# Performance work log

Measured on AMD Instinct MI355X. Metric: run time of the kernel, lower is better.

Reference implementation:

```python
import jax, jax.numpy as jnp
import numpy as np

# Hyperparameters matching init_kwargs
DIM = 1024
HEADS = 16
MEM_HIDDEN = 512
FF_DIM = 4096
CHUNK = 128
NPERSIST = 16
ALPHA = 0.02
THETA = 0.1
ETA = 0.9
B, T = 2, 1024


def _mem_read(x, p):
    """DeepMemory forward: 2-layer MLP dim->hidden->dim with SiLU between."""
    W1, b1, W2, b2 = p
    h = jax.nn.silu(x @ W1.T + b1)
    return h @ W2.T + b2


def setup_inputs() -> dict:
    key = jax.random.key(0)
    ks = jax.random.split(key, 16)
    s = 0.02  # weight init scale
    return {
        "x": jax.random.normal(ks[0], (B, T, DIM), jnp.float32),
        "Wqkv": jax.random.normal(ks[1], (3 * DIM, DIM), jnp.float32) * s,
        "mW1": jax.random.normal(ks[2], (MEM_HIDDEN, DIM), jnp.float32) * s,
        "mb1": jnp.zeros((MEM_HIDDEN,), jnp.float32),
        "mW2": jax.random.normal(ks[3], (DIM, MEM_HIDDEN), jnp.float32) * s,
        "mb2": jnp.zeros((DIM,), jnp.float32),
        "P": jax.random.normal(ks[4], (1, NPERSIST, DIM), jnp.float32),
        "Wqkv_attn": jax.random.normal(ks[5], (3 * DIM, DIM), jnp.float32) * s,
        "Wo": jax.random.normal(ks[6], (DIM, DIM), jnp.float32) * s,
        "ffW1": jax.random.normal(ks[7], (FF_DIM, DIM), jnp.float32) * s,
        "ffb1": jnp.zeros((FF_DIM,), jnp.float32),
        "ffW2": jax.random.normal(ks[8], (DIM, FF_DIM), jnp.float32) * s,
        "ffb2": jnp.zeros((DIM,), jnp.float32),
    }


def reference(x, Wqkv, mW1, mb1, mW2, mb2, P, Wqkv_attn, Wo, ffW1, ffb1, ffW2, ffb2):
    Bb, Tt, D = x.shape
    nC = Tt // CHUNK

    # shared qkv projection (bias-free Linear)
    qkv = x @ Wqkv.T                       # [B,T,3D]
    K = qkv[..., D:2 * D]
    V = qkv[..., 2 * D:]

    # chunked test-time memory writes: k,v are detached in the torch code
    Kc = jax.lax.stop_gradient(K).reshape(Bb, nC, CHUNK, D).transpose(1, 0, 2, 3)  # [nC,B,C,D]
    Vc = jax.lax.stop_gradient(V).reshape(Bb, nC, CHUNK, D).transpose(1, 0, 2, 3)

    params0 = tuple(jax.lax.stop_gradient(p) for p in (mW1, mb1, mW2, mb2))
    mom0 = tuple(jnp.zeros_like(p) for p in params0)

    def loss_fn(p, k, v):
        return jnp.mean((_mem_read(k, p) - v) ** 2)

    def step(carry, kv):
        p, m = carry
        k, v = kv
        g = jax.grad(loss_fn)(p, k, v)
        # momentum: s = eta*s - theta*g ; weight: w = (1-alpha)*w + s
        m = tuple(ETA * mi - THETA * gi for mi, gi in zip(m, g))
        p = tuple((1.0 - ALPHA) * pi + mi for pi, mi in zip(p, m))
        return (p, m), None

    (pf, _), _ = jax.lax.scan(step, (params0, mom0), (Kc, Vc))
    pf = jax.lax.stop_gradient(pf)  # fast weights are buffers (non-differentiable)

    # memory readout tokens for the whole segment
    Q = qkv[..., :D]
    mem_tok = _mem_read(Q, pf)             # [B,T,D]

    # concatenate persistent + memory + input tokens
    tokens = jnp.concatenate([jnp.broadcast_to(P, (Bb, NPERSIST, D)), mem_tok, x], axis=1)
    N = tokens.shape[1]                    # NPERSIST + 2T
    dh = D // HEADS

    # causal multi-head attention over the concatenated sequence
    aqkv = tokens @ Wqkv_attn.T            # [B,N,3D]
    q, k, v = jnp.split(aqkv, 3, axis=-1)
    to_heads = lambda t: t.reshape(Bb, N, HEADS, dh).transpose(0, 2, 1, 3)
    q, k, v = to_heads(q), to_heads(k), to_heads(v)
    scores = jnp.einsum('bhnd,bhmd->bhnm', q, k) / jnp.sqrt(jnp.float32(dh))
    causal = jnp.tril(jnp.ones((N, N), bool))
    scores = jnp.where(causal, scores, jnp.float32(-1e9))
    attn = jax.nn.softmax(scores, axis=-1)
    o = jnp.einsum('bhnm,bhmd->bhnd', attn, v).transpose(0, 2, 1, 3).reshape(Bb, N, D)
    y = o @ Wo.T

    # feed-forward (no residual in source)
    y = jax.nn.gelu(y @ ffW1.T + ffb1) @ ffW2.T + ffb2

    # drop persistent + memory tokens, gate by a fresh memory read
    out = y[:, NPERSIST + Tt:, :]          # [B,T,D]
    newQ = (out @ Wqkv.T)[..., :D]
    return out * _mem_read(newQ, pf)
```

## Files before the change

### kernel.cpp

```cpp
#include <hip/hip_runtime.h>
#include <math.h>

#define BATCH 2
#define TSEQ 1024
#define DIMD 1024
#define NPERS 16
#define NCH 8
#define NTOK 2064
#define ETA_C 0.9f
#define THETA_C 0.1f
#define ALPHA_C 0.02f

typedef __attribute__((ext_vector_type(4))) float f32x4;
typedef __attribute__((ext_vector_type(8))) short s16x8;
typedef unsigned short u16;

__device__ __forceinline__ u16 f2bf(float f) {
    unsigned int u = __float_as_uint(f);
    return (u16)((u + 0x7fffu + ((u >> 16) & 1u)) >> 16);
}
__device__ __forceinline__ float bf2f(u16 h) { return __uint_as_float(((unsigned)h) << 16); }
__device__ __forceinline__ void split2(float v, u16& h, u16& l) {
    h = f2bf(v); l = f2bf(v - bf2f(h));
}

static const size_t oRA = 0;
static const size_t oRB = 50724864;
static const size_t oRC = 67633152;
static const size_t oRD = 80216064;
static const size_t oRE = 96993280;
static const size_t oRF = 109576192;
static const size_t oRG = 113770496;
static const size_t oRH = 117970944;

static const size_t PW1 = 0, PB1 = 524288, PW2 = 524800, PB2 = 1049088, PSZ = 1050112;

__device__ __forceinline__ void gload_lds16(const u16* g, u16* l) {
    __builtin_amdgcn_global_load_lds(
        (const __attribute__((address_space(1))) unsigned int*)g,
        (__attribute__((address_space(3))) unsigned int*)l, 16, 0, 0);
}

__device__ __forceinline__ void xcd_swizzle(int& bx, int& by) {
    int gx = gridDim.x, nwg = gx * gridDim.y;
    int lid = blockIdx.y * gx + blockIdx.x;
    int t = lid;
    if ((nwg & 7) == 0) {
        int q = nwg >> 3;
        t = (lid & 7) * q + (lid >> 3);
    }
    bx = t % gx; by = t / gx;
}

__device__ __forceinline__ void stage_tile(const u16* sp, u16* buf, int rbase,
                                           int M, int clampM, int K, int k0,
                                           int wid, int lane) {
    const int lr = lane >> 2, lc = lane & 3;
    #pragma unroll
    for (int i = 0; i < 8; ++i) {
        int r = i * 16 + lr;
        int gr = rbase + r;
        if (clampM && gr >= M) gr = M - 1;
        int g = lc ^ ((r >> 1) & 3);
        gload_lds16(sp + (size_t)gr * K + k0 + g * 8, buf + wid * 4096 + i * 512);
    }
}

__device__ __forceinline__ void stage_tile64(const u16* sp, u16* buf, int rbase,
                                             int K, int k0, int wid, int lane) {
    const int lr = lane >> 3, lc = lane & 7;
    #pragma unroll
    for (int i = 0; i < 16; ++i) {
        int r = i * 8 + lr;
        int gr = rbase + r;
        int g = lc ^ (r & 7);
        gload_lds16(sp + (size_t)gr * K + k0 + g * 8, buf + wid * 8192 + i * 512);
    }
}

template<int ACTF, int WF32, int WSPLIT, int PARTIAL>
__global__ __launch_bounds__(256)
void gemm_mfma_k(const u16* __restrict__ Ah, const u16* __restrict__ Al,
                 const u16* __restrict__ Wh, const u16* __restrict__ Wl,
                 float* __restrict__ C, u16* __restrict__ Chi, u16* __restrict__ Clo,
                 int M, int N, int K, const float* __restrict__ bias)
{
    __shared__ u16 lds[2][16384];
    const int tid = threadIdx.x;
    const int lane = tid & 63, wid = tid >> 6;
    const int wm = wid >> 1, wn = wid & 1;
    int bx, by; xcd_swizzle(bx, by);
    const int row0 = by * 128, col0 = bx * 128;

    const u16* sp = (wid == 0) ? Ah : (wid == 1) ? Al : (wid == 2) ? Wh : Wl;
    const int rbase = (wid < 2) ? row0 : col0;
    const int clampM = (wid < 2) ? 1 : 0;

    f32x4 acc[4][4] = {};
    const int frow = lane & 15, kblk = lane >> 4;

    int kbeg = 0, kend = K;
    if (PARTIAL) {
        int Kseg = K / gridDim.z;
        kbeg = blockIdx.z * Kseg;
        kend = kbeg + Kseg;
    }
    const int nt = (kend - kbeg) >> 5;

    stage_tile(sp, lds[0], rbase, M, clampM, K, kbeg, wid, lane);

    for (int t = 0; t < nt; ++t) {
        __syncthreads();
        if (t + 1 < nt)
            stage_tile(sp, lds[(t + 1) & 1], rbase, M, clampM, K, kbeg + ((t + 1) << 5), wid, lane);
        const u16* cb = lds[t & 1];

        s16x8 bh[4], bl[4];
        #pragma unroll
        for (int ni = 0; ni < 4; ++ni) {
            int br = wn * 64 + ni * 16 + frow;
            int pc = kblk ^ ((br >> 1) & 3);
            bh[ni] = *(const s16x8*)&cb[2 * 4096 + br * 32 + pc * 8];
            bl[ni] = *(const s16x8*)&cb[3 * 4096 + br * 32 + pc * 8];
        }
        #pragma unroll
        for (int mi = 0; mi < 4; ++mi) {
            int ar = wm * 64 + mi * 16 + frow;
            int pc = kblk ^ ((ar >> 1) & 3);
            s16x8 ah = *(const s16x8*)&cb[0 * 4096 + ar * 32 + pc * 8];
            s16x8 al = *(const s16x8*)&cb[1 * 4096 + ar * 32 + pc * 8];
            #pragma unroll
            for (int ni = 0; ni < 4; ++ni) {
                acc[mi][ni] = __builtin_amdgcn_mfma_f32_16x16x32_bf16(ah, bh[ni], acc[mi][ni], 0, 0, 0);
                acc[mi][ni] = __builtin_amdgcn_mfma_f32_16x16x32_bf16(ah, bl[ni], acc[mi][ni], 0, 0, 0);
                acc[mi][ni] = __builtin_amdgcn_mfma_f32_16x16x32_bf16(al, bh[ni], acc[mi][ni], 0, 0, 0);
            }
        }
    }

    const int erow = (lane >> 4) * 4, ecol = lane & 15;
    #pragma unroll
    for (int mi = 0; mi < 4; ++mi) {
        #pragma unroll
        for (int ni = 0; ni < 4; ++ni) {
            int c = col0 + wn * 64 + ni * 16 + ecol;
            float bv = (!PARTIAL && bias) ? bias[c] : 0.f;
            #pragma unroll
            for (int reg = 0; reg < 4; ++reg) {
                int r = row0 + wm * 64 + mi * 16 + erow + reg;
                if (r >= M) continue;
                float v = acc[mi][ni][reg] + bv;
                if (PARTIAL) {
                    C[((size_t)blockIdx.z * M + r) * N + c] = v;
                    continue;
                }
                if (ACTF == 1) v = v / (1.f + __expf(-v));
                else if (ACTF == 2) {
                    float u = 0.7978845608028654f * (v + 0.044715f * v * v * v);
                    v = 0.5f * v * (1.f + tanhf(u));
                }
                size_t o = (size_t)r * N + c;
                if (WF32) C[o] = v;
                if (WSPLIT) { u16 h, l; split2(v, h, l); Chi[o] = h; Clo[o] = l; }
            }
        }
    }
}

template<int ACTF, int WF32, int WSPLIT>
__global__ __launch_bounds__(256)
void reduce_k(const float* __restrict__ Cp, int S,
              float* __restrict__ C, u16* __restrict__ Chi, u16* __restrict__ Clo,
              const float* __restrict__ bias, int M, int N)
{
    int i = blockIdx.x * 256 + threadIdx.x;
    int n4 = (int)((size_t)M * N / 4);
    if (i >= n4) return;
    size_t off = (size_t)i * 4;
    float4 v = *(const float4*)&Cp[off];
    for (int z = 1; z < S; ++z) {
        float4 u = *(const float4*)&Cp[(size_t)z * M * N + off];
        v.x += u.x; v.y += u.y; v.z += u.z; v.w += u.w;
    }
    int c = (int)(off % N);
    float vv[4] = {v.x, v.y, v.z, v.w};
    #pragma unroll
    for (int j = 0; j < 4; ++j) {
        float w = vv[j];
        if (bias) w += bias[c + j];
        if (ACTF == 1) w = w / (1.f + __expf(-w));
        else if (ACTF == 2) {
            float u = 0.7978845608028654f * (w + 0.044715f * w * w * w);
            w = 0.5f * w * (1.f + tanhf(u));
        }
        if (WF32) C[off + j] = w;
        if (WSPLIT) { u16 h, l; split2(w, h, l); Chi[off + j] = h; Clo[off + j] = l; }
    }
}

static void gemm_mfma(hipStream_t s, int act, int wf32, int wsplit,
                      const u16* Ah, const u16* Al, const u16* Wh, const u16* Wl,
                      float* C, u16* Ch, u16* Cl, int M, int N, int K, const float* bias)
{
    dim3 g(N / 128, (M + 127) / 128), b(256);
    if (act == 0 && wf32 == 1 && wsplit == 0)
        gemm_mfma_k<0,1,0,0><<<g,b,0,s>>>(Ah,Al,Wh,Wl,C,Ch,Cl,M,N,K,bias);
    else if (act == 0 && wf32 == 1 && wsplit == 1)
        gemm_mfma_k<0,1,1,0><<<g,b,0,s>>>(Ah,Al,Wh,Wl,C,Ch,Cl,M,N,K,bias);
    else if (act == 0 && wf32 == 0 && wsplit == 1)
        gemm_mfma_k<0,0,1,0><<<g,b,0,s>>>(Ah,Al,Wh,Wl,C,Ch,Cl,M,N,K,bias);
    else if (act == 1)
        gemm_mfma_k<1,0,1,0><<<g,b,0,s>>>(Ah,Al,Wh,Wl,C,Ch,Cl,M,N,K,bias);
    else
        gemm_mfma_k<2,0,1,0><<<g,b,0,s>>>(Ah,Al,Wh,Wl,C,Ch,Cl,M,N,K,bias);
}

static void gemm_mfma_sk(hipStream_t s, int act, int wf32, int wsplit,
                         const u16* Ah, const u16* Al, const u16* Wh, const u16* Wl,
                         float* C, u16* Ch, u16* Cl, int M, int N, int K,
                         const float* bias, int S, float* part)
{
    if (S <= 1) { gemm_mfma(s, act, wf32, wsplit, Ah, Al, Wh, Wl, C, Ch, Cl, M, N, K, bias); return; }
    dim3 g(N / 128, (M + 127) / 128, S), b(256);
    gemm_mfma_k<0,0,0,1><<<g,b,0,s>>>(Ah,Al,Wh,Wl,part,nullptr,nullptr,M,N,K,nullptr);
    int n4 = (int)((size_t)M * N / 4);
    dim3 rg((n4 + 255) / 256), rb(256);
    if (act == 0 && wf32 == 1 && wsplit == 0)
        reduce_k<0,1,0><<<rg,rb,0,s>>>(part, S, C, Ch, Cl, bias, M, N);
    else if (act == 0 && wf32 == 1 && wsplit == 1)
        reduce_k<0,1,1><<<rg,rb,0,s>>>(part, S, C, Ch, Cl, bias, M, N);
    else if (act == 0 && wf32 == 0 && wsplit == 1)
        reduce_k<0,0,1><<<rg,rb,0,s>>>(part, S, C, Ch, Cl, bias, M, N);
    else if (act == 1)
        reduce_k<1,0,1><<<rg,rb,0,s>>>(part, S, C, Ch, Cl, bias, M, N);
    else
        reduce_k<2,0,1><<<rg,rb,0,s>>>(part, S, C, Ch, Cl, bias, M, N);
}

template<int MODE>
__device__ __forceinline__ void scan_body(u16* lds, int bx, int by,
                 const u16* __restrict__ Ah, const u16* __restrict__ Al,
                 const u16* __restrict__ Wh, const u16* __restrict__ Wl,
                 float* __restrict__ C, u16* __restrict__ Chi, u16* __restrict__ Clo,
                 u16* __restrict__ ChiT, u16* __restrict__ CloT,
                 const float* __restrict__ Zf, const float* __restrict__ add,
                 const float* __restrict__ bias, float* __restrict__ CP,
                 int M, int N, int K, float alpha)
{
    const int tid = threadIdx.x;
    const int lane = tid & 63, wid = tid >> 6;
    const int wm = wid >> 1, wn = wid & 1;
    const int row0 = by * 128, col0 = bx * 128;

    const u16* sp = (wid == 0) ? Ah : (wid == 1) ? Al : (wid == 2) ? Wh : Wl;
    const int rbase = (wid < 2) ? row0 : col0;

    f32x4 acc[4][4] = {};
    const int frow = lane & 15, kblk = lane >> 4;
    const int nt = K >> 6;

    stage_tile64(sp, lds, rbase, K, 0, wid, lane);

    for (int t = 0; t < nt; ++t) {
        __syncthreads();
        if (t + 1 < nt)
            stage_tile64(sp, lds + (((t + 1) & 1) << 15), rbase, K, (t + 1) << 6, wid, lane);
        const u16* cb = lds + ((t & 1) << 15);

        #pragma unroll
        for (int s = 0; s < 2; ++s) {
            s16x8 bh[4], bl[4];
            #pragma unroll
            for (int ni = 0; ni < 4; ++ni) {
                int br = wn * 64 + ni * 16 + frow;
                int pc = (s * 4 + kblk) ^ (br & 7);
                bh[ni] = *(const s16x8*)&cb[2 * 8192 + br * 64 + pc * 8];
                bl[ni] = *(const s16x8*)&cb[3 * 8192 + br * 64 + pc * 8];
            }
            #pragma unroll
            for (int mi = 0; mi < 4; ++mi) {
                int ar = wm * 64 + mi * 16 + frow;
                int pc = (s * 4 + kblk) ^ (ar & 7);
                s16x8 ah = *(const s16x8*)&cb[0 * 8192 + ar * 64 + pc * 8];
                s16x8 al = *(const s16x8*)&cb[1 * 8192 + ar * 64 + pc * 8];
                #pragma unroll
                for (int ni = 0; ni < 4; ++ni) {
                    acc[mi][ni] = __builtin_amdgcn_mfma_f32_16x16x32_bf16(ah, bh[ni], acc[mi][ni], 0, 0, 0);
                    acc[mi][ni] = __builtin_amdgcn_mfma_f32_16x16x32_bf16(ah, bl[ni], acc[mi][ni], 0, 0, 0);
                    acc[mi][ni] = __builtin_amdgcn_mfma_f32_16x16x32_bf16(al, bh[ni], acc[mi][ni], 0, 0, 0);
                }
            }
        }
    }

    const int erow = (lane >> 4) * 4, ecol = lane & 15;
    float csum[4] = {0.f, 0.f, 0.f, 0.f};
    #pragma unroll
    for (int mi = 0; mi < 4; ++mi) {
        #pragma unroll
        for (int ni = 0; ni < 4; ++ni) {
            int c = col0 + wn * 64 + ni * 16 + ecol;
            #pragma unroll
            for (int reg = 0; reg < 4; ++reg) {
                int r = row0 + wm * 64 + mi * 16 + erow + reg;
                float v = acc[mi][ni][reg];
                size_t o = (size_t)r * N + c;
                if (MODE == 1) {
                    v += bias[c];
                    C[o] = v;
                    float hv = v / (1.f + __expf(-v));
                    u16 h, l; split2(hv, h, l);
                    Chi[o] = h; Clo[o] = l;
                    size_t ot = (size_t)c * M + r;
                    ChiT[ot] = h; CloT[ot] = l;
                } else if (MODE == 2) {
                    v += bias[c] - add[o];
                    u16 h, l; split2(v, h, l);
                    Chi[o] = h; Clo[o] = l;
                    size_t ot = (size_t)c * M + r;
                    ChiT[ot] = h; CloT[ot] = l;
                    csum[ni] += v;
                } else if (MODE == 3) {
                    C[o] = alpha * v;
                } else {
                    v *= alpha;
                    float z = Zf[o];
                    float sg = 1.f / (1.f + __expf(-z));
                    v *= sg * (1.f + z * (1.f - sg));
                    u16 h, l; split2(v, h, l);
                    size_t ot = (size_t)c * M + r;
                    ChiT[ot] = h; CloT[ot] = l;
                    csum[ni] += v;
                }
            }
        }
    }
    if (MODE == 2 || MODE == 4) {
        #pragma unroll
        for (int ni = 0; ni < 4; ++ni) {
            float s = csum[ni];
            s += __shfl_xor(s, 16);
            s += __shfl_xor(s, 32);
            if ((lane >> 4) == 0) {
                int c = col0 + wn * 64 + ni * 16 + ecol;
                float w = (MODE == 2) ? alpha * s : s;
                CP[(size_t)(by * 2 + wm) * N + c] = w;
            }
        }
    }
}

template<int MODE>
__global__ __launch_bounds__(256)
void gemm_scan_k(const u16* __restrict__ Ah, const u16* __restrict__ Al,
                 const u16* __restrict__ Wh, const u16* __restrict__ Wl,
                 float* __restrict__ C, u16* __restrict__ Chi, u16* __restrict__ Clo,
                 u16* __restrict__ ChiT, u16* __restrict__ CloT,
                 const float* __restrict__ Zf, const float* __restrict__ add,
                 const float* __restrict__ bias, float* __restrict__ CP,
                 int M, int N, int K, float alpha)
{
    __shared__ u16 lds[2][32768];
    int bx, by; xcd_swizzle(bx, by);
    scan_body<MODE>(&lds[0][0], bx, by, Ah, Al, Wh, Wl, C, Chi, Clo, ChiT, CloT,
                    Zf, add, bias, CP, M, N, K, alpha);
}

__global__ __launch_bounds__(256)
void gemm_scan_pair_k(const u16* __restrict__ rTh, const u16* __restrict__ rTl,
                      const u16* __restrict__ hTh, const u16* __restrict__ hTl,
                      float* __restrict__ gW2,
                      const u16* __restrict__ rh_, const u16* __restrict__ rl_,
                      const u16* __restrict__ w2th, const u16* __restrict__ w2tl,
                      u16* __restrict__ dhTh, u16* __restrict__ dhTl,
                      const float* __restrict__ z1, float* __restrict__ cp1, float cs)
{
    __shared__ u16 lds[2][32768];
    if (blockIdx.y < 8) {
        scan_body<3>(&lds[0][0], blockIdx.x, blockIdx.y, rTh, rTl, hTh, hTl,
                     gW2, nullptr, nullptr, nullptr, nullptr, nullptr, nullptr,
                     nullptr, nullptr, 1024, 512, 256, cs);
    } else {
        scan_body<4>(&lds[0][0], blockIdx.x, blockIdx.y - 8, rh_, rl_, w2th, w2tl,
                     nullptr, nullptr, nullptr, dhTh, dhTl, z1, nullptr,
                     nullptr, cp1, 256, 512, 1024, cs);
    }
}

__global__ void cvt_split_k(const float* __restrict__ in, u16* __restrict__ hi,
                            u16* __restrict__ lo, int n4) {
    int i = blockIdx.x * 256 + threadIdx.x;
    if (i >= n4) return;
    float4 v = *(const float4*)&in[(size_t)i * 4];
    u16 h0,l0,h1,l1,h2,l2,h3,l3;
    split2(v.x,h0,l0); split2(v.y,h1,l1); split2(v.z,h2,l2); split2(v.w,h3,l3);
    ushort4 hv = {h0,h1,h2,h3}, lv = {l0,l1,l2,l3};
    *(ushort4*)&hi[(size_t)i * 4] = hv;
    *(ushort4*)&lo[(size_t)i * 4] = lv;
}
__global__ void transpose_split_k(const float* __restrict__ in, u16* __restrict__ outh,
                                  u16* __restrict__ outl, int R, int C) {
    __shared__ float t[32][33];
    const int c0 = blockIdx.x * 32, r0 = blockIdx.y * 32;
    const size_t zoff = (size_t)blockIdx.z * R * C;
    const int tx = threadIdx.x & 31, ty = threadIdx.x >> 5;
    #pragma unroll
    for (int p = 0; p < 4; ++p) {
        int r = ty + p * 8;
        t[r][tx] = in[zoff + (size_t)(r0 + r) * C + c0 + tx];
    }
    __syncthreads();
    #pragma unroll
    for (int p = 0; p < 4; ++p) {
        int cc = ty + p * 8;
        float v = t[tx][cc];
        u16 h, l; split2(v, h, l);
        size_t o = zoff + (size_t)(c0 + cc) * R + r0 + tx;
        outh[o] = h; outl[o] = l;
    }
}
__global__ void update3_k(float* __restrict__ p, float* __restrict__ mo,
                          const float* __restrict__ g,
                          const float* __restrict__ cp1, const float* __restrict__ cp2,
                          u16* __restrict__ w1h, u16* __restrict__ w1l,
                          u16* __restrict__ w2h, u16* __restrict__ w2l,
                          u16* __restrict__ w2th, u16* __restrict__ w2tl, int n) {
    int i = blockIdx.x * 256 + threadIdx.x;
    if (i >= n) return;
    float gi;
    if (i < 524288) gi = g[i];
    else if (i < 524800) {
        int j = i - 524288;
        gi = cp1[j] + cp1[512 + j] + cp1[1024 + j] + cp1[1536 + j];
    } else if (i < 1049088) gi = g[i];
    else {
        int j = i - 1049088;
        gi = cp2[j] + cp2[1024 + j] + cp2[2048 + j] + cp2[3072 + j];
    }
    float m = ETA_C * mo[i] - THETA_C * gi;
    mo[i] = m;
    float pv = (1.f - ALPHA_C) * p[i] + m;
    p[i] = pv;
    if (i < 524288) {
        u16 h, l; split2(pv, h, l); w1h[i] = h; w1l[i] = l;
    } else if (i >= 524800 && i < 1049088) {
        int j = i - 524800;
        u16 h, l; split2(pv, h, l);
        w2h[j] = h; w2l[j] = l;
        int tj = (j & 511) * 1024 + (j >> 9);
        w2th[tj] = h; w2tl[tj] = l;
    }
}
__global__ void extractqkv2_k(const float* __restrict__ qkv, u16* __restrict__ Qh,
                              u16* __restrict__ Ql, float* __restrict__ Kb,
                              float* __restrict__ Vb) {
    size_t idx = (size_t)blockIdx.x * 256 + threadIdx.x;
    int m = (int)(idx / 3072), col = (int)(idx % 3072);
    int b = m >> 10, t = m & 1023;
    float v = qkv[idx];
    if (col < 1024) {
        size_t o = (size_t)m * 1024 + col;
        u16 h, l; split2(v, h, l); Qh[o] = h; Ql[o] = l;
    } else {
        int d = col & 1023;
        int ch = t >> 7, r = t & 127;
        size_t o = ((size_t)((ch * 2 + b) * 128 + r)) * 1024 + d;
        if (col < 2048) Kb[o] = v; else Vb[o] = v;
    }
}
__global__ void tokens_split_k(const float* __restrict__ P, const float* __restrict__ memtok,
                               const float* __restrict__ x, u16* __restrict__ th,
                               u16* __restrict__ tl) {
    size_t idx = (size_t)blockIdx.x * 256 + threadIdx.x;
    int d = (int)(idx & 1023);
    int n = (int)((idx >> 10) % NTOK);
    int b = (int)(idx / ((size_t)NTOK * 1024));
    float v;
    if (n < NPERS)            v = P[(size_t)n * 1024 + d];
    else if (n < NPERS + TSEQ) v = memtok[((size_t)b * TSEQ + (n - NPERS)) * 1024 + d];
    else                      v = x[((size_t)b * TSEQ + (n - NPERS - TSEQ)) * 1024 + d];
    u16 h, l; split2(v, h, l); th[idx] = h; tl[idx] = l;
}
__global__ void mul_k(const float* __restrict__ a, const float* __restrict__ b,
                      float* __restrict__ o, int n) {
    int i = blockIdx.x * 256 + threadIdx.x;
    if (i < n) o[i] = a[i] * b[i];
}

__global__ void prep_q_k(const float* __restrict__ aqkv, u16* __restrict__ Qh,
                         u16* __restrict__ Ql) {
    size_t idx = (size_t)blockIdx.x * 256 + threadIdx.x;
    int d = (int)(idx & 63);
    int row = (int)((idx >> 6) & 1023);
    int h = (int)((idx >> 16) & 15);
    int b = (int)(idx >> 20);
    float v = 0.125f * aqkv[((size_t)b * NTOK + NPERS + TSEQ + row) * 3072 + h * 64 + d];
    u16 hh, ll; split2(v, hh, ll);
    Qh[idx] = hh; Ql[idx] = ll;
}
__global__ void prep_kk_k(const float* __restrict__ aqkv, u16* __restrict__ Kh,
                          u16* __restrict__ Kl) {
    size_t idx = (size_t)blockIdx.x * 256 + threadIdx.x;
    int d = (int)(idx & 63);
    int n = (int)((idx >> 6) % NTOK);
    int t = (int)(idx / (64 * NTOK));
    int h = t & 15, b = t >> 4;
    float v = aqkv[((size_t)b * NTOK + n) * 3072 + 1024 + h * 64 + d];
    u16 hh, ll; split2(v, hh, ll);
    Kh[idx] = hh; Kl[idx] = ll;
}
__global__ void prep_vt_k(const float* __restrict__ aqkv, u16* __restrict__ Vt) {
    __shared__ float t[64][65];
    const int nt = blockIdx.x, h = blockIdx.y, b = blockIdx.z;
    const int j0 = nt * 64;
    const int lx = threadIdx.x & 63, rg = threadIdx.x >> 6;
    #pragma unroll
    for (int p = 0; p < 16; ++p) {
        int r = rg * 16 + p;
        int n = j0 + r;
        t[r][lx] = (n < NTOK) ? aqkv[((size_t)b * NTOK + n) * 3072 + 2048 + h * 64 + lx] : 0.f;
    }
    __syncthreads();
    #pragma unroll
    for (int p = 0; p < 16; ++p) {
        int d = rg * 16 + p;
        int n = j0 + lx;
        if (n < NTOK)
            Vt[((size_t)(b * 16 + h) * 64 + d) * NTOK + n] = f2bf(t[lx][d]);
    }
}

__global__ __launch_bounds__(256)
void flash_part_k(const u16* __restrict__ Qsh, const u16* __restrict__ Qsl,
                  const u16* __restrict__ Ksh, const u16* __restrict__ Ksl,
                  const u16* __restrict__ Vts, float* __restrict__ Of,
                  float* __restrict__ Mf, float* __restrict__ Lf)
{
    __shared__ u16 lds[20480];
    u16* KH = lds;            u16* KL = lds + 4096;
    u16* VT = lds + 8192;
    u16* PH = lds + 12288;    u16* PL = lds + 16384;

    int lid = blockIdx.x + (blockIdx.y << 4) + (blockIdx.z << 8);
    int t1024 = ((lid & 7) << 7) | (lid >> 3);
    const int qt = t1024 & 15, h = (t1024 >> 4) & 15;
    const int zb = t1024 >> 8;
    const int b = zb >> 1, z = zb & 1;

    const int tid = threadIdx.x;
    const int lane = tid & 63, wid = tid >> 6;
    const int fr = lane & 15, kq = lane >> 4;
    const int bh = b * 16 + h;
    const int q0c = qt * 64;
    const int q0a = NPERS + TSEQ + q0c;
    const int ntile = ((q0a + 63) >> 6) + 1;
    const int half = ntile >> 1;
    const int jt0 = z ? half : 0;
    const int jt1 = z ? ntile : half;
    const int l8 = lane & 7, lr8 = lane >> 3;

    auto stageKV = [&](int jt) {
        const int j0 = jt * 64;
        #pragma unroll
        for (int jj = 0; jj < 6; ++jj) {
            int j = wid * 6 + jj;
            int buf = j >> 3, i8 = j & 7;
            if (buf < 2) {
                int row = i8 * 8 + lr8;
                int grow = j0 + row; if (grow > NTOK - 1) grow = NTOK - 1;
                int c = l8 ^ (row & 7);
                const u16* src = (buf == 0 ? Ksh : Ksl) +
                                 (((size_t)bh * NTOK + grow) << 6) + c * 8;
                gload_lds16(src, (buf == 0 ? KH : KL) + i8 * 512);
            } else {
                int d = i8 * 8 + lr8;
                int c = l8 ^ (d & 7);
                int col = j0 + c * 8; if (col > NTOK - 8) col = NTOK - 8;
                const u16* src = Vts + ((size_t)bh * 64 + d) * NTOK + col;
                gload_lds16(src, VT + i8 * 512);
            }
        }
    };

    s16x8 qh[2], ql[2];
    {
        const size_t qrow = ((size_t)bh * 1024 + q0c + wid * 16 + fr) << 6;
        #pragma unroll
        for (int kb = 0; kb < 2; ++kb) {
            qh[kb] = *(const s16x8*)&Qsh[qrow + (size_t)(kb * 4 + kq) * 8];
            ql[kb] = *(const s16x8*)&Qsl[qrow + (size_t)(kb * 4 + kq) * 8];
        }
    }

    f32x4 Oa[4] = {};
    float mrow[4], lrow[4];
    #pragma unroll
    for (int r = 0; r < 4; ++r) { mrow[r] = -INFINITY; lrow[r] = 0.f; }

    for (int jt = jt0; jt < jt1; ++jt) {
        const int j0 = jt * 64;
        stageKV(jt);
        __syncthreads();

        f32x4 sacc[4] = {};
        __builtin_amdgcn_s_setprio(1);
        #pragma unroll
        for (int nt = 0; nt < 4; ++nt) {
            #pragma unroll
            for (int kb = 0; kb < 2; ++kb) {
                int br = nt * 16 + fr;
                int sl = (kb * 4 + kq) ^ (fr & 7);
                s16x8 kh = *(const s16x8*)&KH[br * 64 + sl * 8];
                s16x8 kl = *(const s16x8*)&KL[br * 64 + sl * 8];
                sacc[nt] = __builtin_amdgcn_mfma_f32_16x16x32_bf16(qh[kb], kh, sacc[nt], 0, 0, 0);
                sacc[nt] = __builtin_amdgcn_mfma_f32_16x16x32_bf16(ql[kb], kh, sacc[nt], 0, 0, 0);
                sacc[nt] = __builtin_amdgcn_mfma_f32_16x16x32_bf16(qh[kb], kl, sacc[nt], 0, 0, 0);
            }
        }
        __builtin_amdgcn_s_setprio(0);

        #pragma unroll
        for (int r = 0; r < 4; ++r) {
            const int qloc = kq * 4 + r;
            const int qi = q0a + wid * 16 + qloc;
            float sv[4], tmax = -INFINITY;
            #pragma unroll
            for (int nt = 0; nt < 4; ++nt) {
                int kj = j0 + nt * 16 + fr;
                sv[nt] = (kj <= qi) ? sacc[nt][r] : -INFINITY;
                tmax = fmaxf(tmax, sv[nt]);
            }
            #pragma unroll
            for (int off = 1; off < 16; off <<= 1)
                tmax = fmaxf(tmax, __shfl_xor(tmax, off));
            float mnew = fmaxf(mrow[r], tmax);
            float scale = __expf(mrow[r] - mnew);
            float psum = 0.f;
            float p4[4];
            #pragma unroll
            for (int nt = 0; nt < 4; ++nt) { p4[nt] = __expf(sv[nt] - mnew); psum += p4[nt]; }
            #pragma unroll
            for (int off = 1; off < 16; off <<= 1)
                psum += __shfl_xor(psum, off);
            lrow[r] = lrow[r] * scale + psum;
            mrow[r] = mnew;
            #pragma unroll
            for (int dt = 0; dt < 4; ++dt) Oa[dt][r] *= scale;
            const int prow = wid * 16 + qloc;
            #pragma unroll
            for (int nt = 0; nt < 4; ++nt) {
                u16 ph, pl; split2(p4[nt], ph, pl);
                int col = nt * 16 + fr;
                int sl = (col >> 3) ^ (qloc & 7);
                int off = prow * 64 + sl * 8 + (col & 7);
                PH[off] = ph; PL[off] = pl;
            }
        }

        __builtin_amdgcn_s_setprio(1);
        #pragma unroll
        for (int kb = 0; kb < 2; ++kb) {
            int pr = wid * 16 + fr;
            int sl = (kb * 4 + kq) ^ (fr & 7);
            s16x8 pa = *(const s16x8*)&PH[pr * 64 + sl * 8];
            s16x8 pb = *(const s16x8*)&PL[pr * 64 + sl * 8];
            #pragma unroll
            for (int dt = 0; dt < 4; ++dt) {
                int vr = dt * 16 + fr;
                s16x8 vb = *(const s16x8*)&VT[vr * 64 + sl * 8];
                Oa[dt] = __builtin_amdgcn_mfma_f32_16x16x32_bf16(pa, vb, Oa[dt], 0, 0, 0);
                Oa[dt] = __builtin_amdgcn_mfma_f32_16x16x32_bf16(pb, vb, Oa[dt], 0, 0, 0);
            }
        }
        __builtin_amdgcn_s_setprio(0);
        __syncthreads();
    }

    const size_t obase = ((((size_t)z * 2 + b) * 16 + h) * 16 + qt) * 4096;
    const size_t mlb   = ((((size_t)z * 2 + b) * 16 + h) * 16 + qt) * 64;
    #pragma unroll
    for (int r = 0; r < 4; ++r) {
        int rl = wid * 16 + kq * 4 + r;
        if (fr == 0) { Mf[mlb + rl] = mrow[r]; Lf[mlb + rl] = lrow[r]; }
        #pragma unroll
        for (int dt = 0; dt < 4; ++dt)
            Of[obase + (size_t)rl * 64 + dt * 16 + fr] = Oa[dt][r];
    }
}

__global__ __launch_bounds__(256)
void flash_merge_k(const float* __restrict__ Of, const float* __restrict__ Mf,
                   const float* __restrict__ Lf, u16* __restrict__ oh, u16* __restrict__ ol)
{
    const int qt = blockIdx.x, h = blockIdx.y, b = blockIdx.z;
    const int tid = threadIdx.x;
    const int row = tid >> 2, quad = tid & 3;
    const size_t b0 = ((((size_t)0 * 2 + b) * 16 + h) * 16 + qt) * 4096 + (size_t)row * 64;
    const size_t b1 = ((((size_t)1 * 2 + b) * 16 + h) * 16 + qt) * 4096 + (size_t)row * 64;
    const size_t m0i = ((((size_t)0 * 2 + b) * 16 + h) * 16 + qt) * 64 + row;
    const size_t m1i = ((((size_t)1 * 2 + b) * 16 + h) * 16 + qt) * 64 + row;
    float m0 = Mf[m0i], m1 = Mf[m1i], l0 = Lf[m0i], l1 = Lf[m1i];
    float m = fmaxf(m0, m1);
    float e0 = __expf(m0 - m), e1 = __expf(m1 - m);
    float inv = 1.f / (l0 * e0 + l1 * e1);
    const size_t orow = ((size_t)(b * 1024 + qt * 64 + row)) * 1024 + h * 64;
    #pragma unroll
    for (int i = 0; i < 4; ++i) {
        int col = quad * 16 + i * 4;
        float4 v0 = *(const float4*)&Of[b0 + col];
        float4 v1 = *(const float4*)&Of[b1 + col];
        float o0 = (v0.x * e0 + v1.x * e1) * inv;
        float o1 = (v0.y * e0 + v1.y * e1) * inv;
        float o2 = (v0.z * e0 + v1.z * e1) * inv;
        float o3 = (v0.w * e0 + v1.w * e1) * inv;
        u16 h0,l0_,h1,l1_,h2,l2_,h3,l3_;
        split2(o0,h0,l0_); split2(o1,h1,l1_); split2(o2,h2,l2_); split2(o3,h3,l3_);
        ushort4 hv = {h0,h1,h2,h3}, lv = {l0_,l1_,l2_,l3_};
        *(ushort4*)&oh[orow + col] = hv;
        *(ushort4*)&ol[orow + col] = lv;
    }
}

extern "C" void kernel_launch(void* const* d_in, const int* in_sizes, int n_in,
                              void* d_out, int out_size, void* d_ws, size_t ws_size,
                              hipStream_t stream)
{
    const float* x     = (const float*)d_in[0];
    const float* Wqkv  = (const float*)d_in[1];
    const float* mW1   = (const float*)d_in[2];
    const float* mb1   = (const float*)d_in[3];
    const float* mW2   = (const float*)d_in[4];
    const float* mb2   = (const float*)d_in[5];
    const float* Pp    = (const float*)d_in[6];
    const float* Wqa   = (const float*)d_in[7];
    const float* Wo    = (const float*)d_in[8];
    const float* ffW1  = (const float*)d_in[9];
    const float* ffb1  = (const float*)d_in[10];
    const float* ffW2  = (const float*)d_in[11];
    const float* ffb2  = (const float*)d_in[12];
    char* wsb = (char*)d_ws;
    float* outp = (float*)d_out;

    float* qkv   = (float*)(wsb + oRA);
    float* z1    = (float*)(wsb + oRA);
    float* grd   = (float*)(wsb + oRA + 3145728);
    float* cp2   = (float*)(wsb + oRA + 7346176);
    float* cp1   = (float*)(wsb + oRA + 7362560);
    u16* hh_     = (u16*)(wsb + oRA + 8388608);
    u16* hl_     = (u16*)(wsb + oRA + 8650752);
    u16* hTh     = (u16*)(wsb + oRA + 9437184);
    u16* hTl     = (u16*)(wsb + oRA + 9699328);
    u16* rh_     = (u16*)(wsb + oRA + 10485760);
    u16* rl_     = (u16*)(wsb + oRA + 11010048);
    u16* rTh     = (u16*)(wsb + oRA + 11534336);
    u16* rTl     = (u16*)(wsb + oRA + 12058624);
    u16* dhTh    = (u16*)(wsb + oRA + 12582912);
    u16* dhTl    = (u16*)(wsb + oRA + 12845056);
    u16* kcTh    = (u16*)(wsb + oRA + 16777216);
    u16* kcTl    = (u16*)(wsb + oRA + 20971520);
    float* aqkv  = (float*)(wsb + oRA);
    float* Of    = (float*)(wsb + oRA);
    float* Mf    = (float*)(wsb + oRA + 33554432);
    float* Lf    = (float*)(wsb + oRA + 34078720);
    u16* Woh     = (u16*)(wsb + oRA);
    u16* Wol     = (u16*)(wsb + oRA + 2097152);
    u16* ffhh    = (u16*)(wsb + oRA);
    u16* ffhl    = (u16*)(wsb + oRA + 16777216);
    u16* outbh   = (u16*)(wsb + oRA + 33554432);
    u16* outbl   = (u16*)(wsb + oRA + 37748736);
    u16* newQh   = (u16*)(wsb + oRA);
    u16* newQl   = (u16*)(wsb + oRA + 4194304);
    u16* hzh     = (u16*)(wsb + oRA + 8388608);
    u16* hzl     = (u16*)(wsb + oRA + 10485760);
    float* memq  = (float*)(wsb + oRA + 12582912);
    float* partA0 = (float*)(wsb + oRA);
    float* partA1 = (float*)(wsb + oRA + 4194304);
    float* partA2 = (float*)(wsb + oRA + 16777216);
    float* Kb    = (float*)(wsb + oRB);
    float* Vb    = (float*)(wsb + oRB + 8388608);
    u16* tokh    = (u16*)(wsb + oRB);
    u16* tokl    = (u16*)(wsb + oRB + 8454144);
    u16* oh      = (u16*)(wsb + oRB);
    u16* ol      = (u16*)(wsb + oRB + 4194304);
    u16* fVth    = (u16*)(wsb + oRB + 8388608);
    u16* y1h     = (u16*)(wsb + oRB + 8388608);
    u16* y1l     = (u16*)(wsb + oRB + 12582912);
    float* partB = (float*)(wsb + oRB);
    u16* xh      = (u16*)(wsb + oRC);
    u16* xl      = (u16*)(wsb + oRC + 4194304);
    float* mom   = (float*)(wsb + oRC);
    u16* pW2Th   = (u16*)(wsb + oRC + 5242880);
    u16* pW2Tl   = (u16*)(wsb + oRC + 6291456);
    u16* Wqah    = (u16*)(wsb + oRC);
    u16* Wqal    = (u16*)(wsb + oRC + 6291456);
    u16* fKl     = (u16*)(wsb + oRC);
    u16* Qh      = (u16*)(wsb + oRD);
    u16* Ql      = (u16*)(wsb + oRD + 4194304);
    u16* kchh    = (u16*)(wsb + oRD + 8388608);
    u16* kchl    = (u16*)(wsb + oRD + 12582912);
    u16* t1h     = (u16*)(wsb + oRD + 8388608);
    u16* t1l     = (u16*)(wsb + oRD + 10485760);
    float* memtok= (float*)(wsb + oRD);
    u16* fKh     = (u16*)(wsb + oRD);
    u16* ffW1h   = (u16*)(wsb + oRD);
    u16* ffW1l   = (u16*)(wsb + oRD + 8388608);
    u16* ffW2h   = (u16*)(wsb + oRD);
    u16* ffW2l   = (u16*)(wsb + oRD + 8388608);
    u16* Wqkvh   = (u16*)(wsb + oRE);
    u16* Wqkvl   = (u16*)(wsb + oRE + 6291456);
    u16* pW1h    = (u16*)(wsb + oRF);
    u16* pW1l    = (u16*)(wsb + oRF + 1048576);
    u16* pW2h    = (u16*)(wsb + oRF + 2097152);
    u16* pW2l    = (u16*)(wsb + oRF + 3145728);
    float* par   = (float*)(wsb + oRG);
    float* outb  = (float*)(wsb + oRH);
    u16* fQh     = (u16*)(wsb + oRH);
    u16* fQl     = (u16*)(wsb + oRH + 4194304);

    hipMemcpyAsync(par + PW1, mW1, 524288 * sizeof(float), hipMemcpyDeviceToDevice, stream);
    hipMemcpyAsync(par + PB1, mb1, 512 * sizeof(float), hipMemcpyDeviceToDevice, stream);
    hipMemcpyAsync(par + PW2, mW2, 524288 * sizeof(float), hipMemcpyDeviceToDevice, stream);
    hipMemcpyAsync(par + PB2, mb2, 1024 * sizeof(float), hipMemcpyDeviceToDevice, stream);

    cvt_split_k<<<2048, 256, 0, stream>>>(x, xh, xl, 524288);
    cvt_split_k<<<3072, 256, 0, stream>>>(Wqkv, Wqkvh, Wqkvl, 786432);
    gemm_mfma(stream, 0, 1, 0, xh, xl, Wqkvh, Wqkvl, qkv, nullptr, nullptr, 2048, 3072, 1024, nullptr);
    extractqkv2_k<<<24576, 256, 0, stream>>>(qkv, Qh, Ql, Kb, Vb);

    hipMemsetAsync(mom, 0, PSZ * sizeof(float), stream);
    cvt_split_k<<<2048, 256, 0, stream>>>(Kb, kchh, kchl, 524288);
    transpose_split_k<<<dim3(32, 8, 8), 256, 0, stream>>>(Kb, kcTh, kcTl, 256, 1024);
    cvt_split_k<<<512, 256, 0, stream>>>(par + PW1, pW1h, pW1l, 131072);
    cvt_split_k<<<512, 256, 0, stream>>>(par + PW2, pW2h, pW2l, 131072);
    transpose_split_k<<<dim3(16, 32, 1), 256, 0, stream>>>(par + PW2, pW2Th, pW2Tl, 1024, 512);

    const float cs = 2.f / (float)(BATCH * 128 * DIMD);
    for (int c = 0; c < NCH; ++c) {
        const u16* kch = kchh + (size_t)c * 262144;
        const u16* kcl = kchl + (size_t)c * 262144;
        const u16* kth = kcTh + (size_t)c * 262144;
        const u16* ktl = kcTl + (size_t)c * 262144;
        const float* vc = Vb + (size_t)c * 262144;
        gemm_scan_k<1><<<dim3(4, 2), 256, 0, stream>>>(kch, kcl, pW1h, pW1l,
            z1, hh_, hl_, hTh, hTl, nullptr, nullptr, par + PB1, nullptr, 256, 512, 1024, 1.f);
        gemm_scan_k<2><<<dim3(8, 2), 256, 0, stream>>>(hh_, hl_, pW2h, pW2l,
            nullptr, rh_, rl_, rTh, rTl, nullptr, vc, par + PB2, cp2, 256, 1024, 512, cs);
        gemm_scan_pair_k<<<dim3(4, 10), 256, 0, stream>>>(rTh, rTl, hTh, hTl, grd + PW2,
            rh_, rl_, pW2Th, pW2Tl, dhTh, dhTl, z1, cp1, cs);
        gemm_scan_k<3><<<dim3(8, 4), 256, 0, stream>>>(dhTh, dhTl, kth, ktl,
            grd + PW1, nullptr, nullptr, nullptr, nullptr, nullptr, nullptr, nullptr, nullptr,
            512, 1024, 256, 1.f);
        update3_k<<<4102, 256, 0, stream>>>(par, mom, grd, cp1, cp2,
            pW1h, pW1l, pW2h, pW2l, pW2Th, pW2Tl, (int)PSZ);
    }

    gemm_mfma_sk(stream, 1, 0, 1, Qh, Ql, pW1h, pW1l, nullptr, t1h, t1l,
                 2048, 512, 1024, par + PB1, 4, partA2);
    gemm_mfma_sk(stream, 0, 1, 0, t1h, t1l, pW2h, pW2l, memtok, nullptr, nullptr,
                 2048, 1024, 512, par + PB2, 2, partA0);

    tokens_split_k<<<16512, 256, 0, stream>>>(Pp, memtok, x, tokh, tokl);
    cvt_split_k<<<3072, 256, 0, stream>>>(Wqa, Wqah, Wqal, 786432);
    gemm_mfma(stream, 0, 1, 0, tokh, tokl, Wqah, Wqal, aqkv, nullptr, nullptr, 4128, 3072, 1024, nullptr);

    prep_q_k<<<8192, 256, 0, stream>>>(aqkv, fQh, fQl);
    prep_kk_k<<<16512, 256, 0, stream>>>(aqkv, fKh, fKl);
    prep_vt_k<<<dim3(33, 16, 2), 256, 0, stream>>>(aqkv, fVth);

    flash_part_k<<<dim3(16, 16, 4), 256, 0, stream>>>(fQh, fQl, fKh, fKl, fVth, Of, Mf, Lf);
    flash_merge_k<<<dim3(16, 16, 2), 256, 0, stream>>>(Of, Mf, Lf, oh, ol);

    cvt_split_k<<<1024, 256, 0, stream>>>(Wo, Woh, Wol, 262144);
    gemm_mfma_sk(stream, 0, 0, 1, oh, ol, Woh, Wol, nullptr, y1h, y1l,
                 2048, 1024, 1024, nullptr, 2, partA1);
    cvt_split_k<<<4096, 256, 0, stream>>>(ffW1, ffW1h, ffW1l, 1048576);
    gemm_mfma(stream, 2, 0, 1, y1h, y1l, ffW1h, ffW1l, nullptr, ffhh, ffhl, 2048, 4096, 1024, ffb1);
    cvt_split_k<<<4096, 256, 0, stream>>>(ffW2, ffW2h, ffW2l, 1048576);
    gemm_mfma_sk(stream, 0, 1, 1, ffhh, ffhl, ffW2h, ffW2l, outb, outbh, outbl,
                 2048, 1024, 4096, ffb2, 2, partB);

    gemm_mfma_sk(stream, 0, 0, 1, outbh, outbl, Wqkvh, Wqkvl, nullptr, newQh, newQl,
                 2048, 1024, 1024, nullptr, 2, partB);
    gemm_mfma_sk(stream, 1, 0, 1, newQh, newQl, pW1h, pW1l, nullptr, hzh, hzl,
                 2048, 512, 1024, par + PB1, 4, partB);
    gemm_mfma_sk(stream, 0, 1, 0, hzh, hzl, pW2h, pW2l, memq, nullptr, nullptr,
                 2048, 1024, 512, par + PB2, 2, partB);
    mul_k<<<8192, 256, 0, stream>>>(outb, memq, outp, 2097152);
}
```

Measured before the change: 1.427 ms.

## Fuse QKV projection epilogues with head/chunk layout and bf16 split writes

Two new GEMM kernels write their outputs straight into the layouts later stages consume. The shared QKV GEMM emits split Q, chunked and transposed K, and chunked V, which replaces the extract, convert and transpose kernels. The attention QKV GEMM emits scaled per-head Q, per-head K and transposed V, which replaces the three prep kernels. This removes the fp32 intermediate round trips and several launches, at the cost of scattered, poorly coalesced stores in the epilogues and a reshuffled workspace layout.

```diff
diff --git a/kernel.cpp b/kernel.cpp
--- a/kernel.cpp
+++ b/kernel.cpp
@@ -78,6 +78,42 @@
     }
 }
 
+__device__ __forceinline__ void mm_loop32(u16 lds[2][16384],
+                const u16* sp, int rbase, int M, int clampM, int K,
+                int kbeg, int kend, int wid, int lane, int wm, int wn,
+                f32x4 acc[4][4]) {
+    const int frow = lane & 15, kblk = lane >> 4;
+    const int nt = (kend - kbeg) >> 5;
+    stage_tile(sp, lds[0], rbase, M, clampM, K, kbeg, wid, lane);
+    for (int t = 0; t < nt; ++t) {
+        __syncthreads();
+        if (t + 1 < nt)
+            stage_tile(sp, lds[(t + 1) & 1], rbase, M, clampM, K, kbeg + ((t + 1) << 5), wid, lane);
+        const u16* cb = lds[t & 1];
+        s16x8 bh[4], bl[4];
+        #pragma unroll
+        for (int ni = 0; ni < 4; ++ni) {
+            int br = wn * 64 + ni * 16 + frow;
+            int pc = kblk ^ ((br >> 1) & 3);
+            bh[ni] = *(const s16x8*)&cb[2 * 4096 + br * 32 + pc * 8];
+            bl[ni] = *(const s16x8*)&cb[3 * 4096 + br * 32 + pc * 8];
+        }
+        #pragma unroll
+        for (int mi = 0; mi < 4; ++mi) {
+            int ar = wm * 64 + mi * 16 + frow;
+            int pc = kblk ^ ((ar >> 1) & 3);
+            s16x8 ah = *(const s16x8*)&cb[0 * 4096 + ar * 32 + pc * 8];
+            s16x8 al = *(const s16x8*)&cb[1 * 4096 + ar * 32 + pc * 8];
+            #pragma unroll
+            for (int ni = 0; ni < 4; ++ni) {
+                acc[mi][ni] = __builtin_amdgcn_mfma_f32_16x16x32_bf16(ah, bh[ni], acc[mi][ni], 0, 0, 0);
+                acc[mi][ni] = __builtin_amdgcn_mfma_f32_16x16x32_bf16(ah, bl[ni], acc[mi][ni], 0, 0, 0);
+                acc[mi][ni] = __builtin_amdgcn_mfma_f32_16x16x32_bf16(al, bh[ni], acc[mi][ni], 0, 0, 0);
+            }
+        }
+    }
+}
+
 template<int ACTF, int WF32, int WSPLIT, int PARTIAL>
 __global__ __launch_bounds__(256)
 void gemm_mfma_k(const u16* __restrict__ Ah, const u16* __restrict__ Al,
@@ -91,52 +127,17 @@
     const int wm = wid >> 1, wn = wid & 1;
     int bx, by; xcd_swizzle(bx, by);
     const int row0 = by * 128, col0 = bx * 128;
-
     const u16* sp = (wid == 0) ? Ah : (wid == 1) ? Al : (wid == 2) ? Wh : Wl;
     const int rbase = (wid < 2) ? row0 : col0;
     const int clampM = (wid < 2) ? 1 : 0;
-
     f32x4 acc[4][4] = {};
-    const int frow = lane & 15, kblk = lane >> 4;
-
     int kbeg = 0, kend = K;
     if (PARTIAL) {
         int Kseg = K / gridDim.z;
         kbeg = blockIdx.z * Kseg;
         kend = kbeg + Kseg;
     }
-    const int nt = (kend - kbeg) >> 5;
-
-    stage_tile(sp, lds[0], rbase, M, clampM, K, kbeg, wid, lane);
-
-    for (int t = 0; t < nt; ++t) {
-        __syncthreads();
-        if (t + 1 < nt)
-            stage_tile(sp, lds[(t + 1) & 1], rbase, M, clampM, K, kbeg + ((t + 1) << 5), wid, lane);
-        const u16* cb = lds[t & 1];
-
-        s16x8 bh[4], bl[4];
-        #pragma unroll
-        for (int ni = 0; ni < 4; ++ni) {
-            int br = wn * 64 + ni * 16 + frow;
-            int pc = kblk ^ ((br >> 1) & 3);
-            bh[ni] = *(const s16x8*)&cb[2 * 4096 + br * 32 + pc * 8];
-            bl[ni] = *(const s16x8*)&cb[3 * 4096 + br * 32 + pc * 8];
-        }
-        #pragma unroll
-        for (int mi = 0; mi < 4; ++mi) {
-            int ar = wm * 64 + mi * 16 + frow;
-            int pc = kblk ^ ((ar >> 1) & 3);
-            s16x8 ah = *(const s16x8*)&cb[0 * 4096 + ar * 32 + pc * 8];
-            s16x8 al = *(const s16x8*)&cb[1 * 4096 + ar * 32 + pc * 8];
-            #pragma unroll
-            for (int ni = 0; ni < 4; ++ni) {
-                acc[mi][ni] = __builtin_amdgcn_mfma_f32_16x16x32_bf16(ah, bh[ni], acc[mi][ni], 0, 0, 0);
-                acc[mi][ni] = __builtin_amdgcn_mfma_f32_16x16x32_bf16(ah, bl[ni], acc[mi][ni], 0, 0, 0);
-                acc[mi][ni] = __builtin_amdgcn_mfma_f32_16x16x32_bf16(al, bh[ni], acc[mi][ni], 0, 0, 0);
-            }
-        }
-    }
+    mm_loop32(lds, sp, rbase, M, clampM, K, kbeg, kend, wid, lane, wm, wn, acc);
 
     const int erow = (lane >> 4) * 4, ecol = lane & 15;
     #pragma unroll
@@ -162,6 +163,113 @@
                 size_t o = (size_t)r * N + c;
                 if (WF32) C[o] = v;
                 if (WSPLIT) { u16 h, l; split2(v, h, l); Chi[o] = h; Clo[o] = l; }
+            }
+        }
+    }
+}
+
+__global__ __launch_bounds__(256)
+void gemm_qkv_k(const u16* __restrict__ Ah, const u16* __restrict__ Al,
+                const u16* __restrict__ Wh, const u16* __restrict__ Wl,
+                u16* __restrict__ Qh, u16* __restrict__ Ql,
+                u16* __restrict__ kch, u16* __restrict__ kcl,
+                u16* __restrict__ kcTh, u16* __restrict__ kcTl,
+                float* __restrict__ Vb, int M, int N, int K)
+{
+    __shared__ u16 lds[2][16384];
+    const int tid = threadIdx.x;
+    const int lane = tid & 63, wid = tid >> 6;
+    const int wm = wid >> 1, wn = wid & 1;
+    int bx, by; xcd_swizzle(bx, by);
+    const int row0 = by * 128, col0 = bx * 128;
+    const u16* sp = (wid == 0) ? Ah : (wid == 1) ? Al : (wid == 2) ? Wh : Wl;
+    const int rbase = (wid < 2) ? row0 : col0;
+    f32x4 acc[4][4] = {};
+    mm_loop32(lds, sp, rbase, M, 0, K, 0, K, wid, lane, wm, wn, acc);
+
+    const int erow = (lane >> 4) * 4, ecol = lane & 15;
+    #pragma unroll
+    for (int mi = 0; mi < 4; ++mi) {
+        #pragma unroll
+        for (int ni = 0; ni < 4; ++ni) {
+            int c = col0 + wn * 64 + ni * 16 + ecol;
+            #pragma unroll
+            for (int reg = 0; reg < 4; ++reg) {
+                int r = row0 + wm * 64 + mi * 16 + erow + reg;
+                float v = acc[mi][ni][reg];
+                int b = r >> 10, t = r & 1023;
+                if (c < 1024) {
+                    size_t o = (size_t)r * 1024 + c;
+                    u16 h, l; split2(v, h, l); Qh[o] = h; Ql[o] = l;
+                } else if (c < 2048) {
+                    int d = c - 1024;
+                    int ch = t >> 7, rr = t & 127;
+                    size_t o = ((size_t)((ch * 2 + b) * 128 + rr)) * 1024 + d;
+                    u16 h, l; split2(v, h, l);
+                    kch[o] = h; kcl[o] = l;
+                    size_t ot = (size_t)ch * 262144 + (size_t)d * 256 + b * 128 + rr;
+                    kcTh[ot] = h; kcTl[ot] = l;
+                } else {
+                    int d = c - 2048;
+                    int ch = t >> 7, rr = t & 127;
+                    Vb[((size_t)((ch * 2 + b) * 128 + rr)) * 1024 + d] = v;
+                }
+            }
+        }
+    }
+}
+
+__global__ __launch_bounds__(256)
+void gemm_aqkv_k(const u16* __restrict__ Ah, const u16* __restrict__ Al,
+                 const u16* __restrict__ Wh, const u16* __restrict__ Wl,
+                 u16* __restrict__ fQh, u16* __restrict__ fQl,
+                 u16* __restrict__ fKh, u16* __restrict__ fKl,
+                 u16* __restrict__ fVt, int M, int N, int K)
+{
+    __shared__ u16 lds[2][16384];
+    const int tid = threadIdx.x;
+    const int lane = tid & 63, wid = tid >> 6;
+    const int wm = wid >> 1, wn = wid & 1;
+    int bx, by; xcd_swizzle(bx, by);
+    const int row0 = by * 128, col0 = bx * 128;
+    const u16* sp = (wid == 0) ? Ah : (wid == 1) ? Al : (wid == 2) ? Wh : Wl;
+    const int rbase = (wid < 2) ? row0 : col0;
+    const int clampM = (wid < 2) ? 1 : 0;
+    f32x4 acc[4][4] = {};
+    mm_loop32(lds, sp, rbase, M, clampM, K, 0, K, wid, lane, wm, wn, acc);
+
+    const int erow = (lane >> 4) * 4, ecol = lane & 15;
+    #pragma unroll
+    for (int mi = 0; mi < 4; ++mi) {
+        #pragma unroll
+        for (int ni = 0; ni < 4; ++ni) {
+            int c = col0 + wn * 64 + ni * 16 + ecol;
+            #pragma unroll
+            for (int reg = 0; reg < 4; ++reg) {
+                int r = row0 + wm * 64 + mi * 16 + erow + reg;
+                if (r >= M) continue;
+                float v = acc[mi][ni][reg];
+                int b = (r >= 2064) ? 1 : 0;
+                int n = r - b * 2064;
+                if (c < 1024) {
+                    if (n >= NPERS + TSEQ) {
+                        int h = c >> 6, d = c & 63;
+                        int row = n - (NPERS + TSEQ);
+                        size_t o = (((size_t)(b * 16 + h)) * 1024 + row) * 64 + d;
+                        u16 hh, ll; split2(0.125f * v, hh, ll);
+                        fQh[o] = hh; fQl[o] = ll;
+                    }
+                } else if (c < 2048) {
+                    int cc = c - 1024;
+                    int h = cc >> 6, d = cc & 63;
+                    size_t o = (((size_t)(b * 16 + h)) * NTOK + n) * 64 + d;
+                    u16 hh, ll; split2(v, hh, ll);
+                    fKh[o] = hh; fKl[o] = ll;
+                } else {
+                    int cc = c - 2048;
+                    int h = cc >> 6, d = cc & 63;
+                    fVt[(((size_t)(b * 16 + h)) * 64 + d) * NTOK + n] = f2bf(v);
+                }
             }
         }
     }
@@ -451,23 +559,6 @@
         w2th[tj] = h; w2tl[tj] = l;
     }
 }
-__global__ void extractqkv2_k(const float* __restrict__ qkv, u16* __restrict__ Qh,
-                              u16* __restrict__ Ql, float* __restrict__ Kb,
-                              float* __restrict__ Vb) {
-    size_t idx = (size_t)blockIdx.x * 256 + threadIdx.x;
-    int m = (int)(idx / 3072), col = (int)(idx % 3072);
-    int b = m >> 10, t = m & 1023;
-    float v = qkv[idx];
-    if (col < 1024) {
-        size_t o = (size_t)m * 1024 + col;
-        u16 h, l; split2(v, h, l); Qh[o] = h; Ql[o] = l;
-    } else {
-        int d = col & 1023;
-        int ch = t >> 7, r = t & 127;
-        size_t o = ((size_t)((ch * 2 + b) * 128 + r)) * 1024 + d;
-        if (col < 2048) Kb[o] = v; else Vb[o] = v;
-    }
-}
 __global__ void tokens_split_k(const float* __restrict__ P, const float* __restrict__ memtok,
                                const float* __restrict__ x, u16* __restrict__ th,
                                u16* __restrict__ tl) {
@@ -485,49 +576,6 @@
                       float* __restrict__ o, int n) {
     int i = blockIdx.x * 256 + threadIdx.x;
     if (i < n) o[i] = a[i] * b[i];
-}
-
-__global__ void prep_q_k(const float* __restrict__ aqkv, u16* __restrict__ Qh,
-                         u16* __restrict__ Ql) {
-    size_t idx = (size_t)blockIdx.x * 256 + threadIdx.x;
-    int d = (int)(idx & 63);
-    int row = (int)((idx >> 6) & 1023);
-    int h = (int)((idx >> 16) & 15);
-    int b = (int)(idx >> 20);
-    float v = 0.125f * aqkv[((size_t)b * NTOK + NPERS + TSEQ + row) * 3072 + h * 64 + d];
-    u16 hh, ll; split2(v, hh, ll);
-    Qh[idx] = hh; Ql[idx] = ll;
-}
-__global__ void prep_kk_k(const float* __restrict__ aqkv, u16* __restrict__ Kh,
-                          u16* __restrict__ Kl) {
-    size_t idx = (size_t)blockIdx.x * 256 + threadIdx.x;
-    int d = (int)(idx & 63);
-    int n = (int)((idx >> 6) % NTOK);
-    int t = (int)(idx / (64 * NTOK));
-    int h = t & 15, b = t >> 4;
-    float v = aqkv[((size_t)b * NTOK + n) * 3072 + 1024 + h * 64 + d];
-    u16 hh, ll; split2(v, hh, ll);
-    Kh[idx] = hh; Kl[idx] = ll;
-}
-__global__ void prep_vt_k(const float* __restrict__ aqkv, u16* __restrict__ Vt) {
-    __shared__ float t[64][65];
-    const int nt = blockIdx.x, h = blockIdx.y, b = blockIdx.z;
-    const int j0 = nt * 64;
-    const int lx = threadIdx.x & 63, rg = threadIdx.x >> 6;
-    #pragma unroll
-    for (int p = 0; p < 16; ++p) {
-        int r = rg * 16 + p;
-        int n = j0 + r;
-        t[r][lx] = (n < NTOK) ? aqkv[((size_t)b * NTOK + n) * 3072 + 2048 + h * 64 + lx] : 0.f;
-    }
-    __syncthreads();
-    #pragma unroll
-    for (int p = 0; p < 16; ++p) {
-        int d = rg * 16 + p;
-        int n = j0 + lx;
-        if (n < NTOK)
-            Vt[((size_t)(b * 16 + h) * 64 + d) * NTOK + n] = f2bf(t[lx][d]);
-    }
 }
 
 __global__ __launch_bounds__(256)
@@ -741,7 +789,6 @@
     char* wsb = (char*)d_ws;
     float* outp = (float*)d_out;
 
-    float* qkv   = (float*)(wsb + oRA);
     float* z1    = (float*)(wsb + oRA);
     float* grd   = (float*)(wsb + oRA + 3145728);
     float* cp2   = (float*)(wsb + oRA + 7346176);
@@ -758,10 +805,11 @@
     u16* dhTl    = (u16*)(wsb + oRA + 12845056);
     u16* kcTh    = (u16*)(wsb + oRA + 16777216);
     u16* kcTl    = (u16*)(wsb + oRA + 20971520);
-    float* aqkv  = (float*)(wsb + oRA);
     float* Of    = (float*)(wsb + oRA);
-    float* Mf    = (float*)(wsb + oRA + 33554432);
-    float* Lf    = (float*)(wsb + oRA + 34078720);
+    float* Mf    = (float*)(wsb + oRA + 16777216);
+    float* Lf    = (float*)(wsb + oRA + 17039360);
+    u16* fVth    = (u16*)(wsb + oRA + 17825792);
+    u16* fKl     = (u16*)(wsb + oRA + 26279936);
     u16* Woh     = (u16*)(wsb + oRA);
     u16* Wol     = (u16*)(wsb + oRA + 2097152);
     u16* ffhh    = (u16*)(wsb + oRA);
@@ -776,13 +824,11 @@
     float* partA0 = (float*)(wsb + oRA);
     float* partA1 = (float*)(wsb + oRA + 4194304);
     float* partA2 = (float*)(wsb + oRA + 16777216);
-    float* Kb    = (float*)(wsb + oRB);
     float* Vb    = (float*)(wsb + oRB + 8388608);
     u16* tokh    = (u16*)(wsb + oRB);
     u16* tokl    = (u16*)(wsb + oRB + 8454144);
     u16* oh      = (u16*)(wsb + oRB);
     u16* ol      = (u16*)(wsb + oRB + 4194304);
-    u16* fVth    = (u16*)(wsb + oRB + 8388608);
     u16* y1h     = (u16*)(wsb + oRB + 8388608);
     u16* y1l     = (u16*)(wsb + oRB + 12582912);
     float* partB = (float*)(wsb + oRB);
@@ -793,7 +839,6 @@
     u16* pW2Tl   = (u16*)(wsb + oRC + 6291456);
     u16* Wqah    = (u16*)(wsb + oRC);
     u16* Wqal    = (u16*)(wsb + oRC + 6291456);
-    u16* fKl     = (u16*)(wsb + oRC);
     u16* Qh      = (u16*)(wsb + oRD);
     u16* Ql      = (u16*)(wsb + oRD + 4194304);
     u16* kchh    = (u16*)(wsb + oRD + 8388608);
@@ -824,12 +869,10 @@
 
     cvt_split_k<<<2048, 256, 0, stream>>>(x, xh, xl, 524288);
     cvt_split_k<<<3072, 256, 0, stream>>>(Wqkv, Wqkvh, Wqkvl, 786432);
-    gemm_mfma(stream, 0, 1, 0, xh, xl, Wqkvh, Wqkvl, qkv, nullptr, nullptr, 2048, 3072, 1024, nullptr);
-    extractqkv2_k<<<24576, 256, 0, stream>>>(qkv, Qh, Ql, Kb, Vb);
+    gemm_qkv_k<<<dim3(24, 16), 256, 0, stream>>>(xh, xl, Wqkvh, Wqkvl,
+        Qh, Ql, kchh, kchl, kcTh, kcTl, Vb, 2048, 3072, 1024);
 
     hipMemsetAsync(mom, 0, PSZ * sizeof(float), stream);
-    cvt_split_k<<<2048, 256, 0, stream>>>(Kb, kchh, kchl, 524288);
-    transpose_split_k<<<dim3(32, 8, 8), 256, 0, stream>>>(Kb, kcTh, kcTl, 256, 1024);
     cvt_split_k<<<512, 256, 0, stream>>>(par + PW1, pW1h, pW1l, 131072);
     cvt_split_k<<<512, 256, 0, stream>>>(par + PW2, pW2h, pW2l, 131072);
     transpose_split_k<<<dim3(16, 32, 1), 256, 0, stream>>>(par + PW2, pW2Th, pW2Tl, 1024, 512);
@@ -861,11 +904,8 @@
 
     tokens_split_k<<<16512, 256, 0, stream>>>(Pp, memtok, x, tokh, tokl);
     cvt_split_k<<<3072, 256, 0, stream>>>(Wqa, Wqah, Wqal, 786432);
-    gemm_mfma(stream, 0, 1, 0, tokh, tokl, Wqah, Wqal, aqkv, nullptr, nullptr, 4128, 3072, 1024, nullptr);
-
-    prep_q_k<<<8192, 256, 0, stream>>>(aqkv, fQh, fQl);
-    prep_kk_k<<<16512, 256, 0, stream>>>(aqkv, fKh, fKl);
-    prep_vt_k<<<dim3(33, 16, 2), 256, 0, stream>>>(aqkv, fVth);
+    gemm_aqkv_k<<<dim3(24, 33), 256, 0, stream>>>(tokh, tokl, Wqah, Wqal,
+        fQh, fQl, fKh, fKl, fVth, 4128, 3072, 1024);
 
     flash_part_k<<<dim3(16, 16, 4), 256, 0, stream>>>(fQh, fQl, fKh, fKl, fVth, Of, Mf, Lf);
     flash_merge_k<<<dim3(16, 16, 2), 256, 0, stream>>>(Of, Mf, Lf, oh, ol);
```

Measured after the change: 1.396 ms. -2.2%, faster.
